# Performance work log

Measured on AMD Instinct MI355X. Metric: run time of the kernel, lower is better.

Reference implementation:

```python
import jax, jax.numpy as jnp
import numpy as np

B, T, C, H = 8, 2048, 1024, 128  # batch, seq, n_embed, head_size

def setup_inputs() -> dict:
    key = jax.random.key(0)
    ks = jax.random.split(key, 6)
    s = 1.0 / np.sqrt(C)
    return {
        "x": jax.random.normal(ks[0], (B, T, C), dtype=jnp.float32),
        "Wk": jax.random.uniform(ks[1], (C, H), minval=-s, maxval=s, dtype=jnp.float32),
        "Wq": jax.random.uniform(ks[2], (C, H), minval=-s, maxval=s, dtype=jnp.float32),
        "Wv": jax.random.uniform(ks[3], (C, H), minval=-s, maxval=s, dtype=jnp.float32),
        "Wp": jax.random.uniform(ks[4], (H, H), minval=-1/np.sqrt(H), maxval=1/np.sqrt(H), dtype=jnp.float32),
        "bp": jax.random.uniform(ks[5], (H,), minval=-1/np.sqrt(H), maxval=1/np.sqrt(H), dtype=jnp.float32),
    }

def reference(x, Wk, Wq, Wv, Wp, bp):
    # x: [B,T,C]; projections are bias-free
    k = x @ Wk  # [B,T,H]
    q = x @ Wq
    v = x @ Wv
    scale = jnp.asarray(H, x.dtype) ** -0.5
    scores = jnp.einsum('bqh,bkh->bqk', q, k) * scale  # [B,T,T]
    causal = jnp.tril(jnp.ones((T, T), dtype=bool))
    scores = jnp.where(causal, scores, jnp.finfo(x.dtype).min)
    w = jax.nn.softmax(scores, axis=-1)
    out = jnp.einsum('bqk,bkh->bqh', w, v)  # [B,T,H]
    return out @ Wp + bp
```

## Files before the change

### kernel.cpp

```cpp
#include <hip/hip_runtime.h>

constexpr int Bz = 8, Tt = 2048, Cc = 1024, Hh = 128;
constexpr int Mrows = Bz * Tt;
constexpr float kScale = 0.08838834764831843f;

typedef float f32x4 __attribute__((ext_vector_type(4)));
typedef short s16x8 __attribute__((ext_vector_type(8)));
typedef short s16x4 __attribute__((ext_vector_type(4)));
typedef unsigned short u16;

static __device__ __forceinline__ u16 f2bf(float f) {
    union { float f; unsigned int u; } c; c.f = f;
    unsigned int u = c.u;
    unsigned int r = (u + 0x7fffu + ((u >> 16) & 1u)) >> 16;
    return (u16)r;
}

__global__ __launch_bounds__(256) void convw_kernel(
    const float* __restrict__ Wq, const float* __restrict__ Wk,
    const float* __restrict__ Wv, const float* __restrict__ Wp,
    u16* __restrict__ wt, u16* __restrict__ wpt)
{
    int i = blockIdx.x * 256 + threadIdx.x;
    if (i < 393216) {
        int z = i >> 17, r = i & 131071;
        int n = r >> 10, k = r & 1023;
        const float* W = (z == 0) ? Wq : (z == 1) ? Wk : Wv;
        wt[i] = f2bf(W[k * Hh + n]);
    } else {
        int r2 = i - 393216;
        int n = r2 >> 7, k = r2 & 127;
        wpt[r2] = f2bf(Wp[k * Hh + n]);
    }
}

__global__ __launch_bounds__(512)
__attribute__((amdgpu_waves_per_eu(2, 4)))
void qkv_fused(
    const float* __restrict__ x, const u16* __restrict__ wt,
    u16* __restrict__ qo, u16* __restrict__ ko, u16* __restrict__ vt)
{
    __shared__ __align__(16) u16 as[64 * 64];

    const int tid  = threadIdx.x;
    const int m0   = blockIdx.x * 64;
    const int lane = tid & 63, wid = tid >> 6;
    const int l15  = lane & 15, l4 = lane >> 4;
    const int bb   = m0 >> 11;
    const int t0   = m0 & 2047;

    f32x4 acc[4][3];
#pragma unroll
    for (int mi = 0; mi < 4; ++mi)
#pragma unroll
        for (int ni = 0; ni < 3; ++ni) {
            f32x4 z4 = {0.f, 0.f, 0.f, 0.f};
            acc[mi][ni] = z4;
        }

    for (int k0 = 0; k0 < Cc; k0 += 64) {
#pragma unroll
        for (int u = 0; u < 2; ++u) {
            int idx = tid + u * 512;
            int m = idx >> 4, kf4 = (idx & 15) * 4;
            float4 xv = *reinterpret_cast<const float4*>(
                &x[(size_t)(m0 + m) * Cc + k0 + kf4]);
            s16x4 bv;
            bv[0] = (short)f2bf(xv.x); bv[1] = (short)f2bf(xv.y);
            bv[2] = (short)f2bf(xv.z); bv[3] = (short)f2bf(xv.w);
            *reinterpret_cast<s16x4*>(&as[m * 64 + (kf4 ^ ((m & 7) << 3))]) = bv;
        }
        s16x8 bfr[3][2];
#pragma unroll
        for (int ni = 0; ni < 3; ++ni) {
            int c = wid * 48 + ni * 16;
            int z = c >> 7, nloc = (c & 127) + l15;
            const u16* wb = wt + (size_t)z * 131072 + (size_t)nloc * 1024 + k0;
#pragma unroll
            for (int ks = 0; ks < 2; ++ks)
                bfr[ni][ks] = *reinterpret_cast<const s16x8*>(&wb[ks * 32 + l4 * 8]);
        }
        __syncthreads();

        s16x8 af[4][2];
#pragma unroll
        for (int mi = 0; mi < 4; ++mi) {
            int r = mi * 16 + l15;
#pragma unroll
            for (int ks = 0; ks < 2; ++ks)
                af[mi][ks] = *reinterpret_cast<const s16x8*>(
                    &as[r * 64 + ((ks * 32 + l4 * 8) ^ ((r & 7) << 3))]);
        }
#pragma unroll
        for (int mi = 0; mi < 4; ++mi)
#pragma unroll
            for (int ni = 0; ni < 3; ++ni)
#pragma unroll
                for (int ks = 0; ks < 2; ++ks)
                    acc[mi][ni] = __builtin_amdgcn_mfma_f32_16x16x32_bf16(
                        af[mi][ks], bfr[ni][ks], acc[mi][ni], 0, 0, 0);
        __syncthreads();
    }

#pragma unroll
    for (int mi = 0; mi < 4; ++mi)
#pragma unroll
        for (int ni = 0; ni < 3; ++ni) {
            int c = wid * 48 + ni * 16;
            int z = c >> 7, colz = (c & 127) + l15;
            if (z < 2) {
                u16* outp = (z == 0) ? qo : ko;
#pragma unroll
                for (int r = 0; r < 4; ++r) {
                    int row = m0 + mi * 16 + l4 * 4 + r;
                    outp[(size_t)row * Hh + colz] = f2bf(acc[mi][ni][r]);
                }
            } else {
                int trow = t0 + mi * 16 + l4 * 4;
                s16x4 pk;
#pragma unroll
                for (int r = 0; r < 4; ++r) pk[r] = (short)f2bf(acc[mi][ni][r]);
                *reinterpret_cast<s16x4*>(
                    &vt[((size_t)bb * Hh + colz) * Tt + trow]) = pk;
            }
        }
}

__global__ __launch_bounds__(256, 2)
void attn_kernel(
    const u16* __restrict__ q, const u16* __restrict__ k,
    const u16* __restrict__ vt, const u16* __restrict__ wpt,
    const float* __restrict__ bp, float* __restrict__ O)
{
    __shared__ __align__(16) char arena[43008];
    u16* ksl = reinterpret_cast<u16*>(arena);
    u16* vsl = reinterpret_cast<u16*>(arena + 16384);
    u16* psl = reinterpret_cast<u16*>(arena + 32768);
    float* Om  = reinterpret_cast<float*>(arena);
    float* ml2 = reinterpret_cast<float*>(arena + 33792);
    u16*   pm  = reinterpret_cast<u16*>(arena + 34304);

    const int tid = threadIdx.x, lane = tid & 63, wid = tid >> 6;
    const int l15 = lane & 15, l4 = lane >> 4;
    const int wq = wid >> 1, half = wid & 1;
    const int bid = blockIdx.x;
    const int b  = bid & 7;
    const int qt = 63 - (bid >> 3);
    const int q0 = qt * 32;
    const int ntiles = (qt + 2) >> 1;

    const u16* qb = q  + (size_t)b * Tt * Hh;
    const u16* kb = k  + (size_t)b * Tt * Hh;
    const u16* vb = vt + (size_t)b * Hh * Tt;

    const int qrow = q0 + wq * 16 + l15;
    s16x8 qf[4];
#pragma unroll
    for (int ks = 0; ks < 4; ++ks)
        qf[ks] = *reinterpret_cast<const s16x8*>(
            &qb[(size_t)qrow * Hh + ks * 32 + l4 * 8]);

    f32x4 o[8];
#pragma unroll
    for (int nh = 0; nh < 8; ++nh) { f32x4 z4 = {0.f,0.f,0.f,0.f}; o[nh] = z4; }
    float mreg = -1e30f, lreg = 0.f;

    const int kr_s  = tid >> 2, kc_s = (tid & 3) * 4;
    const int vh_s  = tid >> 1, vc_s = (tid & 1) * 4;
    u16* ps = psl + wid * 16 * 80;

    for (int j = 0; j < ntiles; ++j) {
        const int kv0 = j * 64;

#pragma unroll
        for (int i = 0; i < 4; ++i) {
            s16x8 tk = *reinterpret_cast<const s16x8*>(
                &kb[(size_t)(kv0 + kr_s) * Hh + (kc_s + i) * 8]);
            *reinterpret_cast<s16x8*>(
                &ksl[kr_s * 128 + (((kc_s + i) * 8) ^ ((kr_s & 7) << 3))]) = tk;
        }
#pragma unroll
        for (int i = 0; i < 4; ++i) {
            s16x8 tv = *reinterpret_cast<const s16x8*>(
                &vb[(size_t)vh_s * Tt + kv0 + (vc_s + i) * 8]);
            *reinterpret_cast<s16x8*>(
                &vsl[vh_s * 64 + (((vc_s + i) * 8) ^ ((vh_s & 7) << 3))]) = tv;
        }
        __syncthreads();

        f32x4 sacc[2];
#pragma unroll
        for (int nf = 0; nf < 2; ++nf) { f32x4 z4 = {0.f,0.f,0.f,0.f}; sacc[nf] = z4; }
#pragma unroll
        for (int nf = 0; nf < 2; ++nf) {
            const int kr = half * 32 + nf * 16 + l15;
#pragma unroll
            for (int ks = 0; ks < 4; ++ks) {
                s16x8 kfrag = *reinterpret_cast<const s16x8*>(
                    &ksl[kr * 128 + ((ks * 32 + l4 * 8) ^ ((kr & 7) << 3))]);
                sacc[nf] = __builtin_amdgcn_mfma_f32_16x16x32_bf16(
                    kfrag, qf[ks], sacc[nf], 0, 0, 0);
            }
        }

        const bool diag = (j == ntiles - 1);
        float pv2[2][4];
#pragma unroll
        for (int nf = 0; nf < 2; ++nf)
#pragma unroll
            for (int r = 0; r < 4; ++r) {
                float s = sacc[nf][r] * kScale;
                if (diag) {
                    int kvg = kv0 + half * 32 + nf * 16 + l4 * 4 + r;
                    if (kvg > qrow) s = -1e30f;
                }
                pv2[nf][r] = s;
            }
        float mx = fmaxf(fmaxf(fmaxf(pv2[0][0], pv2[0][1]), fmaxf(pv2[0][2], pv2[0][3])),
                         fmaxf(fmaxf(pv2[1][0], pv2[1][1]), fmaxf(pv2[1][2], pv2[1][3])));
        mx = fmaxf(mx, __shfl_xor(mx, 16));
        mx = fmaxf(mx, __shfl_xor(mx, 32));
        const float mold = mreg;
        const float mnew = fmaxf(mold, mx);
        const float scl = __expf(mold - mnew);
        mreg = mnew;
        float rs = 0.f;
#pragma unroll
        for (int nf = 0; nf < 2; ++nf)
#pragma unroll
            for (int r = 0; r < 4; ++r) {
                float pp = __expf(pv2[nf][r] - mnew);
                pv2[nf][r] = pp; rs += pp;
            }
        rs += __shfl_xor(rs, 16);
        rs += __shfl_xor(rs, 32);
        lreg = lreg * scl + rs;

        if (!__all(mold == mnew)) {
            float sclr[4];
#pragma unroll
            for (int r = 0; r < 4; ++r) sclr[r] = __shfl(scl, l4 * 4 + r);
#pragma unroll
            for (int nh = 0; nh < 8; ++nh)
#pragma unroll
                for (int r = 0; r < 4; ++r) o[nh][r] *= sclr[r];
        }

#pragma unroll
        for (int nf = 0; nf < 2; ++nf) {
            s16x4 pk4;
#pragma unroll
            for (int r = 0; r < 4; ++r) pk4[r] = (short)f2bf(pv2[nf][r]);
            *reinterpret_cast<s16x4*>(&ps[l15 * 80 + nf * 16 + l4 * 4]) = pk4;
        }
        s16x8 pa = *reinterpret_cast<const s16x8*>(&ps[l15 * 80 + l4 * 8]);

#pragma unroll
        for (int nh = 0; nh < 8; ++nh) {
            const int hr = nh * 16 + l15;
            s16x8 vfrag = *reinterpret_cast<const s16x8*>(
                &vsl[hr * 64 + ((half * 32 + l4 * 8) ^ ((hr & 7) << 3))]);
            o[nh] = __builtin_amdgcn_mfma_f32_16x16x32_bf16(
                pa, vfrag, o[nh], 0, 0, 0);
        }
        __syncthreads();
    }

#pragma unroll
    for (int nh = 0; nh < 8; ++nh)
#pragma unroll
        for (int r = 0; r < 4; ++r)
            Om[((wid * 16) + l4 * 4 + r) * 132 + nh * 16 + l15] = o[nh][r];
    if (lane < 16) {
        ml2[wid * 32 + lane] = mreg;
        ml2[wid * 32 + 16 + lane] = lreg;
    }
    __syncthreads();

    {
        const int row = tid >> 3, ch = tid & 7;
        const int rg = row >> 4, r16 = row & 15;
        const int w0 = rg * 2, w1 = rg * 2 + 1;
        float m0v = ml2[w0 * 32 + r16], m1v = ml2[w1 * 32 + r16];
        float M = fmaxf(m0v, m1v);
        float f0 = __expf(m0v - M), f1 = __expf(m1v - M);
        float L = f0 * ml2[w0 * 32 + 16 + r16] + f1 * ml2[w1 * 32 + 16 + r16];
        float inv = 1.f / L;
        union { u16 u[8]; s16x8 v; } pk0, pk1;
#pragma unroll
        for (int c = 0; c < 8; ++c) {
            float a = f0 * Om[(w0 * 16 + r16) * 132 + ch * 16 + c]
                    + f1 * Om[(w1 * 16 + r16) * 132 + ch * 16 + c];
            pk0.u[c] = f2bf(a * inv);
        }
#pragma unroll
        for (int c = 0; c < 8; ++c) {
            float a = f0 * Om[(w0 * 16 + r16) * 132 + ch * 16 + 8 + c]
                    + f1 * Om[(w1 * 16 + r16) * 132 + ch * 16 + 8 + c];
            pk1.u[c] = f2bf(a * inv);
        }
        *reinterpret_cast<s16x8*>(&pm[row * 136 + ch * 16]) = pk0.v;
        *reinterpret_cast<s16x8*>(&pm[row * 136 + ch * 16 + 8]) = pk1.v;
    }
    __syncthreads();

    {
        const int rg2 = (wid >> 1) * 16;
        const int cg  = (wid & 1) * 64;
        s16x8 af2[4];
#pragma unroll
        for (int ks = 0; ks < 4; ++ks)
            af2[ks] = *reinterpret_cast<const s16x8*>(
                &pm[(rg2 + l15) * 136 + ks * 32 + l4 * 8]);
#pragma unroll
        for (int ng = 0; ng < 4; ++ng) {
            const int ncol = cg + ng * 16 + l15;
            f32x4 pacc = {0.f, 0.f, 0.f, 0.f};
#pragma unroll
            for (int ks = 0; ks < 4; ++ks) {
                s16x8 wf = *reinterpret_cast<const s16x8*>(
                    &wpt[(size_t)ncol * 128 + ks * 32 + l4 * 8]);
                pacc = __builtin_amdgcn_mfma_f32_16x16x32_bf16(
                    af2[ks], wf, pacc, 0, 0, 0);
            }
            float bias = bp[ncol];
#pragma unroll
            for (int r = 0; r < 4; ++r)
                O[((size_t)(b * Tt) + q0 + rg2 + l4 * 4 + r) * Hh + ncol] =
                    pacc[r] + bias;
        }
    }
}

extern "C" void kernel_launch(void* const* d_in, const int* in_sizes, int n_in,
                              void* d_out, int out_size, void* d_ws, size_t ws_size,
                              hipStream_t stream) {
    const float* x  = (const float*)d_in[0];
    const float* Wk = (const float*)d_in[1];
    const float* Wq = (const float*)d_in[2];
    const float* Wv = (const float*)d_in[3];
    const float* Wp = (const float*)d_in[4];
    const float* bp = (const float*)d_in[5];
    float* out = (float*)d_out;

    u16* wtb = (u16*)d_ws;
    u16* wpt = wtb + 393216;
    u16* qw  = wpt + 16384;
    u16* kw  = qw + (size_t)Mrows * Hh;
    u16* vtb = kw + (size_t)Mrows * Hh;

    convw_kernel<<<1600, 256, 0, stream>>>(Wq, Wk, Wv, Wp, wtb, wpt);
    qkv_fused<<<Mrows / 64, 512, 0, stream>>>(x, wtb, qw, kw, vtb);
    attn_kernel<<<512, 256, 0, stream>>>(qw, kw, vtb, wpt, bp, out);
}
```

Before: 96.87 us.

## Split attention KV range in two, merge partials in a separate projection kernel

The attention kernel now processes each query tile in two blocks that each cover half of the key/value tiles, writing unnormalized bf16 partial outputs plus max and sum statistics to workspace. A new merge_proj kernel combines the two partials, normalizes, and applies the output projection and bias. The QKV projection is also retiled from 64 to 32 rows per block, and attention occupancy hints are raised. The intent is to double the grid size and balance causal work across CUs. The cost is an extra launch, extra global traffic for the partials, and additional bf16 rounding of the unnormalized output.

```diff
diff --git a/kernel.cpp b/kernel.cpp
--- a/kernel.cpp
+++ b/kernel.cpp
@@ -14,6 +14,10 @@
     unsigned int u = c.u;
     unsigned int r = (u + 0x7fffu + ((u >> 16) & 1u)) >> 16;
     return (u16)r;
+}
+static __device__ __forceinline__ float bf2f(u16 x) {
+    union { unsigned int u; float f; } c; c.u = ((unsigned int)x) << 16;
+    return c.f;
 }
 
 __global__ __launch_bounds__(256) void convw_kernel(
@@ -34,24 +38,23 @@
     }
 }
 
-__global__ __launch_bounds__(512)
-__attribute__((amdgpu_waves_per_eu(2, 4)))
+__global__ __launch_bounds__(512, 2)
 void qkv_fused(
     const float* __restrict__ x, const u16* __restrict__ wt,
     u16* __restrict__ qo, u16* __restrict__ ko, u16* __restrict__ vt)
 {
-    __shared__ __align__(16) u16 as[64 * 64];
+    __shared__ __align__(16) u16 as[32 * 64];
 
     const int tid  = threadIdx.x;
-    const int m0   = blockIdx.x * 64;
+    const int m0   = blockIdx.x * 32;
     const int lane = tid & 63, wid = tid >> 6;
     const int l15  = lane & 15, l4 = lane >> 4;
     const int bb   = m0 >> 11;
     const int t0   = m0 & 2047;
 
-    f32x4 acc[4][3];
-#pragma unroll
-    for (int mi = 0; mi < 4; ++mi)
+    f32x4 acc[2][3];
+#pragma unroll
+    for (int mi = 0; mi < 2; ++mi)
 #pragma unroll
         for (int ni = 0; ni < 3; ++ni) {
             f32x4 z4 = {0.f, 0.f, 0.f, 0.f};
@@ -59,10 +62,8 @@
         }
 
     for (int k0 = 0; k0 < Cc; k0 += 64) {
-#pragma unroll
-        for (int u = 0; u < 2; ++u) {
-            int idx = tid + u * 512;
-            int m = idx >> 4, kf4 = (idx & 15) * 4;
+        {
+            int m = tid >> 4, kf4 = (tid & 15) * 4;
             float4 xv = *reinterpret_cast<const float4*>(
                 &x[(size_t)(m0 + m) * Cc + k0 + kf4]);
             s16x4 bv;
@@ -82,9 +83,9 @@
         }
         __syncthreads();
 
-        s16x8 af[4][2];
-#pragma unroll
-        for (int mi = 0; mi < 4; ++mi) {
+        s16x8 af[2][2];
+#pragma unroll
+        for (int mi = 0; mi < 2; ++mi) {
             int r = mi * 16 + l15;
 #pragma unroll
             for (int ks = 0; ks < 2; ++ks)
@@ -92,7 +93,7 @@
                     &as[r * 64 + ((ks * 32 + l4 * 8) ^ ((r & 7) << 3))]);
         }
 #pragma unroll
-        for (int mi = 0; mi < 4; ++mi)
+        for (int mi = 0; mi < 2; ++mi)
 #pragma unroll
             for (int ni = 0; ni < 3; ++ni)
 #pragma unroll
@@ -103,7 +104,7 @@
     }
 
 #pragma unroll
-    for (int mi = 0; mi < 4; ++mi)
+    for (int mi = 0; mi < 2; ++mi)
 #pragma unroll
         for (int ni = 0; ni < 3; ++ni) {
             int c = wid * 48 + ni * 16;
@@ -126,28 +127,31 @@
         }
 }
 
-__global__ __launch_bounds__(256, 2)
+__global__ __launch_bounds__(256, 4)
 void attn_kernel(
     const u16* __restrict__ q, const u16* __restrict__ k,
-    const u16* __restrict__ vt, const u16* __restrict__ wpt,
-    const float* __restrict__ bp, float* __restrict__ O)
+    const u16* __restrict__ vt,
+    u16* __restrict__ Opart, float* __restrict__ Mp, float* __restrict__ Lp)
 {
-    __shared__ __align__(16) char arena[43008];
+    __shared__ __align__(16) char arena[37888];
     u16* ksl = reinterpret_cast<u16*>(arena);
     u16* vsl = reinterpret_cast<u16*>(arena + 16384);
     u16* psl = reinterpret_cast<u16*>(arena + 32768);
     float* Om  = reinterpret_cast<float*>(arena);
     float* ml2 = reinterpret_cast<float*>(arena + 33792);
-    u16*   pm  = reinterpret_cast<u16*>(arena + 34304);
 
     const int tid = threadIdx.x, lane = tid & 63, wid = tid >> 6;
     const int l15 = lane & 15, l4 = lane >> 4;
     const int wq = wid >> 1, half = wid & 1;
     const int bid = blockIdx.x;
-    const int b  = bid & 7;
-    const int qt = 63 - (bid >> 3);
+    const int b = bid & 7;
+    const int rest = bid >> 3;
+    const int qt = 63 - (rest >> 1);
+    const int split = rest & 1;
     const int q0 = qt * 32;
-    const int ntiles = (qt + 2) >> 1;
+    const int ntf = (qt + 2) >> 1;
+    const int lo = (ntf * split) >> 1;
+    const int hi = (ntf * (split + 1)) >> 1;
 
     const u16* qb = q  + (size_t)b * Tt * Hh;
     const u16* kb = k  + (size_t)b * Tt * Hh;
@@ -167,9 +171,9 @@
 
     const int kr_s  = tid >> 2, kc_s = (tid & 3) * 4;
     const int vh_s  = tid >> 1, vc_s = (tid & 1) * 4;
-    u16* ps = psl + wid * 16 * 80;
-
-    for (int j = 0; j < ntiles; ++j) {
+    u16* ps = psl + wid * 640;
+
+    for (int j = lo; j < hi; ++j) {
         const int kv0 = j * 64;
 
 #pragma unroll
@@ -203,7 +207,7 @@
             }
         }
 
-        const bool diag = (j == ntiles - 1);
+        const bool diag = (j == ntf - 1);
         float pv2[2][4];
 #pragma unroll
         for (int nf = 0; nf < 2; ++nf)
@@ -251,9 +255,9 @@
             s16x4 pk4;
 #pragma unroll
             for (int r = 0; r < 4; ++r) pk4[r] = (short)f2bf(pv2[nf][r]);
-            *reinterpret_cast<s16x4*>(&ps[l15 * 80 + nf * 16 + l4 * 4]) = pk4;
-        }
-        s16x8 pa = *reinterpret_cast<const s16x8*>(&ps[l15 * 80 + l4 * 8]);
+            *reinterpret_cast<s16x4*>(&ps[l15 * 40 + nf * 16 + l4 * 4]) = pk4;
+        }
+        s16x8 pa = *reinterpret_cast<const s16x8*>(&ps[l15 * 40 + l4 * 8]);
 
 #pragma unroll
         for (int nh = 0; nh < 8; ++nh) {
@@ -285,36 +289,80 @@
         float M = fmaxf(m0v, m1v);
         float f0 = __expf(m0v - M), f1 = __expf(m1v - M);
         float L = f0 * ml2[w0 * 32 + 16 + r16] + f1 * ml2[w1 * 32 + 16 + r16];
-        float inv = 1.f / L;
+        const size_t gm = (size_t)b * Tt + q0 + row;
         union { u16 u[8]; s16x8 v; } pk0, pk1;
 #pragma unroll
         for (int c = 0; c < 8; ++c) {
             float a = f0 * Om[(w0 * 16 + r16) * 132 + ch * 16 + c]
                     + f1 * Om[(w1 * 16 + r16) * 132 + ch * 16 + c];
-            pk0.u[c] = f2bf(a * inv);
+            pk0.u[c] = f2bf(a);
         }
 #pragma unroll
         for (int c = 0; c < 8; ++c) {
             float a = f0 * Om[(w0 * 16 + r16) * 132 + ch * 16 + 8 + c]
                     + f1 * Om[(w1 * 16 + r16) * 132 + ch * 16 + 8 + c];
-            pk1.u[c] = f2bf(a * inv);
-        }
-        *reinterpret_cast<s16x8*>(&pm[row * 136 + ch * 16]) = pk0.v;
-        *reinterpret_cast<s16x8*>(&pm[row * 136 + ch * 16 + 8]) = pk1.v;
+            pk1.u[c] = f2bf(a);
+        }
+        u16* op = Opart + ((size_t)split * Mrows + gm) * 128 + ch * 16;
+        *reinterpret_cast<s16x8*>(op) = pk0.v;
+        *reinterpret_cast<s16x8*>(op + 8) = pk1.v;
+        if (ch == 0) {
+            Mp[split * Mrows + gm] = M;
+            Lp[split * Mrows + gm] = L;
+        }
+    }
+}
+
+__global__ __launch_bounds__(256) void merge_proj(
+    const u16* __restrict__ Opart, const float* __restrict__ Mp,
+    const float* __restrict__ Lp, const u16* __restrict__ wpt,
+    const float* __restrict__ bp, float* __restrict__ O)
+{
+    __shared__ __align__(16) u16 pm[64 * 136];
+    __shared__ float f0s[64], f1s[64], invs[64];
+
+    const int tid = threadIdx.x, lane = tid & 63, wid = tid >> 6;
+    const int l15 = lane & 15, l4 = lane >> 4;
+    const int m0r = blockIdx.x * 64;
+
+    if (tid < 64) {
+        float m0v = Mp[m0r + tid], m1v = Mp[Mrows + m0r + tid];
+        float M = fmaxf(m0v, m1v);
+        float a0 = __expf(m0v - M), a1 = __expf(m1v - M);
+        float L = a0 * Lp[m0r + tid] + a1 * Lp[Mrows + m0r + tid];
+        f0s[tid] = a0; f1s[tid] = a1; invs[tid] = 1.f / L;
     }
     __syncthreads();
 
+#pragma unroll
+    for (int u = 0; u < 4; ++u) {
+        int idx = tid + u * 256;
+        int row = idx >> 4, g = idx & 15;
+        const size_t base = (size_t)(m0r + row) * 128 + g * 8;
+        s16x8 p0 = *reinterpret_cast<const s16x8*>(&Opart[base]);
+        s16x8 p1 = *reinterpret_cast<const s16x8*>(
+            &Opart[(size_t)Mrows * 128 + base]);
+        float a0 = f0s[row], a1 = f1s[row], inv = invs[row];
+        union { u16 u[8]; s16x8 v; } pk;
+#pragma unroll
+        for (int c = 0; c < 8; ++c) {
+            float v0 = bf2f((u16)p0[c]), v1 = bf2f((u16)p1[c]);
+            pk.u[c] = f2bf((a0 * v0 + a1 * v1) * inv);
+        }
+        *reinterpret_cast<s16x8*>(&pm[row * 136 + g * 8]) = pk.v;
+    }
+    __syncthreads();
+
     {
-        const int rg2 = (wid >> 1) * 16;
-        const int cg  = (wid & 1) * 64;
+        const int row2 = wid * 16 + l15;
         s16x8 af2[4];
 #pragma unroll
         for (int ks = 0; ks < 4; ++ks)
             af2[ks] = *reinterpret_cast<const s16x8*>(
-                &pm[(rg2 + l15) * 136 + ks * 32 + l4 * 8]);
-#pragma unroll
-        for (int ng = 0; ng < 4; ++ng) {
-            const int ncol = cg + ng * 16 + l15;
+                &pm[row2 * 136 + ks * 32 + l4 * 8]);
+#pragma unroll
+        for (int ng = 0; ng < 8; ++ng) {
+            const int ncol = ng * 16 + l15;
             f32x4 pacc = {0.f, 0.f, 0.f, 0.f};
 #pragma unroll
             for (int ks = 0; ks < 4; ++ks) {
@@ -326,7 +374,7 @@
             float bias = bp[ncol];
 #pragma unroll
             for (int r = 0; r < 4; ++r)
-                O[((size_t)(b * Tt) + q0 + rg2 + l4 * 4 + r) * Hh + ncol] =
+                O[(size_t)(m0r + wid * 16 + l4 * 4 + r) * Hh + ncol] =
                     pacc[r] + bias;
         }
     }
@@ -348,8 +396,12 @@
     u16* qw  = wpt + 16384;
     u16* kw  = qw + (size_t)Mrows * Hh;
     u16* vtb = kw + (size_t)Mrows * Hh;
+    u16* opart = vtb + (size_t)Mrows * Hh;
+    float* Mpart = (float*)(opart + (size_t)2 * Mrows * Hh);
+    float* Lpart = Mpart + 2 * Mrows;
 
     convw_kernel<<<1600, 256, 0, stream>>>(Wq, Wk, Wv, Wp, wtb, wpt);
-    qkv_fused<<<Mrows / 64, 512, 0, stream>>>(x, wtb, qw, kw, vtb);
-    attn_kernel<<<512, 256, 0, stream>>>(qw, kw, vtb, wpt, bp, out);
-}
+    qkv_fused<<<Mrows / 32, 512, 0, stream>>>(x, wtb, qw, kw, vtb);
+    attn_kernel<<<1024, 256, 0, stream>>>(qw, kw, vtb, opart, Mpart, Lpart);
+    merge_proj<<<Mrows / 64, 256, 0, stream>>>(opart, Mpart, Lpart, wpt, bp, out);
+}
```

Result: no change. 98.50 us (+1.7%).
